# Performance work log

Hardware: AMD Instinct MI355X
Metric: run time of the kernel (lower is better)

The kernel has to match this reference:

```python
import jax, jax.numpy as jnp
import numpy as np

POOL = 7  # adaptive_avg_pool2d output size (7,7)


def _bin_edges(start, length):
    """Adaptive-avg-pool bin boundaries.
    start, length: [N] int32 -> (lo, hi) each [N, POOL] absolute indices,
    matching torch: lo_i = floor(i*L/P), hi_i = ceil((i+1)*L/P).
    """
    i = jnp.arange(POOL, dtype=jnp.int32)
    lo = start[:, None] + (i[None, :] * length[:, None]) // POOL
    hi = start[:, None] + (-((-(i[None, :] + 1)) * length[:, None] // POOL))
    # note: ceil(a/b) = -(-a // b); written below explicitly
    hi = start[:, None] - ((-(i[None, :] + 1) * length[:, None]) // POOL)
    return lo, hi


def roi_adaptive_avg_pool(features, rois):
    """features: [1, C, H, W]; rois: [N, 4] int (x1,y1,x2,y2 inclusive).
    Returns [N, C, POOL, POOL] == torch stack of adaptive_avg_pool2d over
    features[:, :, y1:y2+1, x1:x2+1], vectorized via an integral image.
    """
    B, C, H, W = features.shape  # B == 1 (forced by shared_fcs input dim)
    # integral image with a zero row/col prepended: ii[y, x] = sum over [:y, :x]
    ii = jnp.cumsum(jnp.cumsum(features, axis=2), axis=3)
    ii = jnp.pad(ii, ((0, 0), (0, 0), (1, 0), (1, 0)))[0]  # [C, H+1, W+1]

    x1, y1, x2, y2 = rois[:, 0], rois[:, 1], rois[:, 2], rois[:, 3]
    ys, ye = _bin_edges(y1, y2 - y1 + 1)   # [N, POOL]
    xs, xe = _bin_edges(x1, x2 - x1 + 1)
    Y0, Y1 = ys[:, :, None], ye[:, :, None]   # [N, POOL, 1]
    X0, X1 = xs[:, None, :], xe[:, None, :]   # [N, 1, POOL]

    def gather(Y, X):
        return ii[:, Y, X]  # [C, N, POOL, POOL]

    sums = gather(Y1, X1) - gather(Y0, X1) - gather(Y1, X0) + gather(Y0, X0)
    area = ((Y1 - Y0) * (X1 - X0)).astype(features.dtype)  # [N, POOL, POOL]
    pooled = sums / area[None]                              # [C, N, POOL, POOL]
    return jnp.transpose(pooled, (1, 0, 2, 3))              # [N, C, POOL, POOL]


def setup_inputs() -> dict:
    key = jax.random.key(0)
    ks = jax.random.split(key, 12)
    C, H, W, N, F = 256, 336, 336, 2000, 256
    features = jax.random.normal(ks[0], (1, C, H, W), dtype=jnp.float32)
    # valid small ROIs (shuttlecock-sized), x1<=x2, y1<=y2, in-bounds
    x1 = jax.random.randint(ks[1], (N,), 0, W - 40)
    y1 = jax.random.randint(ks[2], (N,), 0, H - 40)
    bw = jax.random.randint(ks[3], (N,), 4, 40)
    bh = jax.random.randint(ks[4], (N,), 4, 40)
    rois = jnp.stack([x1, y1, jnp.minimum(x1 + bw, W - 1),
                      jnp.minimum(y1 + bh, H - 1)], axis=1).astype(jnp.int32)
    d_in = C * POOL * POOL
    w1 = jax.random.normal(ks[5], (d_in, F), dtype=jnp.float32) * (1.0 / np.sqrt(d_in))
    b1 = jnp.zeros((F,), dtype=jnp.float32)
    w2 = jax.random.normal(ks[6], (F, F), dtype=jnp.float32) * (1.0 / np.sqrt(F))
    b2 = jnp.zeros((F,), dtype=jnp.float32)
    w_cls = jax.random.normal(ks[7], (F, 2), dtype=jnp.float32) * 0.01
    b_cls = jnp.zeros((2,), dtype=jnp.float32)
    w_reg = jax.random.normal(ks[8], (F, 4), dtype=jnp.float32) * 0.001
    b_reg = jnp.zeros((4,), dtype=jnp.float32)
    return {"features": features, "rois": rois, "w1": w1, "b1": b1,
            "w2": w2, "b2": b2, "w_cls": w_cls, "b_cls": b_cls,
            "w_reg": w_reg, "b_reg": b_reg}


def reference(features, rois, w1, b1, w2, b2, w_cls, b_cls, w_reg, b_reg):
    roi_feats = roi_adaptive_avg_pool(features, rois)          # [N, C, 7, 7]
    roi_feats = roi_feats.reshape(roi_feats.shape[0], -1)      # [N, C*49]
    h = jax.nn.relu(roi_feats @ w1 + b1)
    h = jax.nn.relu(h @ w2 + b2)
    cls_score = h @ w_cls + b_cls                              # [N, num_classes+1]
    bbox_pred = h @ w_reg + b_reg                              # [N, 4]
    return (cls_score, bbox_pred)
```

## Files before the change

kernel.cpp:

```cpp
#include <hip/hip_runtime.h>

typedef unsigned int uint;
typedef unsigned short ushort;
typedef __bf16 v8bf __attribute__((ext_vector_type(8)));
typedef float v4f __attribute__((ext_vector_type(4)));

#define CCH 256
#define HH 336
#define WW 336
#define HWSZ (HH*WW)
#define NROI 2000
#define KDIM 12544
#define MPAD 2048
#define SPLITK 14
#define KSP (KDIM/SPLITK)

__device__ __forceinline__ ushort bf16r(float f) {
  uint u = __float_as_uint(f);
  u += 0x7fffu + ((u >> 16) & 1u);
  return (ushort)(u >> 16);
}
__device__ __forceinline__ uint packbf(float a, float b) {
  return (uint)bf16r(a) | ((uint)bf16r(b) << 16);
}

typedef const __attribute__((address_space(1))) uint* gas_t;
typedef __attribute__((address_space(3))) uint* las_t;
__device__ __forceinline__ void async16(const void* g, void* l) {
  __builtin_amdgcn_global_load_lds((gas_t)g, (las_t)l, 16, 0, 0);
}

__global__ __launch_bounds__(256) void k_transpose(const float* __restrict__ f,
                                                   uint* __restrict__ ftu) {
  __shared__ uint T[64 * 132];
  int tid = threadIdx.x;
  int hw0 = blockIdx.x * 64;
  int hwl = tid & 63;
  int cq = tid >> 6;
  int hw = hw0 + hwl;
#pragma unroll 4
  for (int it = 0; it < 32; ++it) {
    int c = it * 8 + cq * 2;
    float a = f[(size_t)c * HWSZ + hw];
    float b = f[(size_t)(c + 1) * HWSZ + hw];
    T[hwl * 132 + it * 4 + cq] = packbf(a, b);
  }
  __syncthreads();
  int co = tid & 31, r = tid >> 5;
#pragma unroll
  for (int i = 0; i < 8; ++i) {
    int hwr = i * 8 + r;
    uint4 v = *(const uint4*)&T[hwr * 132 + co * 4];
    *(uint4*)(ftu + (size_t)(hw0 + hwr) * 128 + co * 4) = v;
  }
}

__global__ __launch_bounds__(256) void k_w1perm(const float* __restrict__ w1,
                                                uint* __restrict__ w1t_u) {
  int bin = blockIdx.x % 49;
  int c0 = (blockIdx.x / 49) * 32;
  __shared__ ushort T[32][258];
  int n = threadIdx.x;
  for (int i = 0; i < 32; ++i)
    T[i][n] = bf16r(w1[(size_t)((c0 + i) * 49 + bin) * 256 + n]);
  __syncthreads();
  int cc = threadIdx.x & 15;
  int nb = threadIdx.x >> 4;
  for (int rep = 0; rep < 16; ++rep) {
    int nn = rep * 16 + nb;
    uint v = (uint)T[2 * cc][nn] | ((uint)T[2 * cc + 1][nn] << 16);
    w1t_u[(size_t)nn * (KDIM / 2) + bin * 128 + c0 / 2 + cc] = v;
  }
}

__global__ __launch_bounds__(256) void k_w2t(const float* __restrict__ w2,
                                             ushort* __restrict__ w2t) {
  int n = blockIdx.x, k = threadIdx.x;
  w2t[n * 256 + k] = bf16r(w2[k * 256 + n]);
}

#define UNPK8(u) do {                                        \
  a[0] += __uint_as_float((u).x << 16);                      \
  a[1] += __uint_as_float((u).x & 0xffff0000u);              \
  a[2] += __uint_as_float((u).y << 16);                      \
  a[3] += __uint_as_float((u).y & 0xffff0000u);              \
  a[4] += __uint_as_float((u).z << 16);                      \
  a[5] += __uint_as_float((u).z & 0xffff0000u);              \
  a[6] += __uint_as_float((u).w << 16);                      \
  a[7] += __uint_as_float((u).w & 0xffff0000u);              \
} while (0)

__global__ __launch_bounds__(448) void k_pool(const int* __restrict__ rois,
                                              const uint4* __restrict__ ft4,
                                              uint4* __restrict__ rf4) {
  int n = blockIdx.x;
  int wv = threadIdx.x >> 6;
  int t = threadIdx.x & 63;
  int co = t & 31, par = t >> 5;
  int x1 = rois[n * 4 + 0], y1 = rois[n * 4 + 1];
  int x2 = rois[n * 4 + 2], y2 = rois[n * 4 + 3];
  int Lw = x2 - x1 + 1, Lh = y2 - y1 + 1;
  int ylo = y1 + (wv * Lh) / 7;
  int yhi = y1 + ((wv + 1) * Lh + 6) / 7;
  int rh = yhi - ylo;
  uint ob = (uint)n * 1568 + (uint)wv * 224 + co;
  for (int b = 0; b < 7; ++b) {
    int lo = x1 + (b * Lw) / 7;
    int hi = x1 + ((b + 1) * Lw + 6) / 7;
    float a[8];
#pragma unroll
    for (int j = 0; j < 8; ++j) a[j] = 0.f;
    for (int y = ylo; y < yhi; ++y) {
      const uint4* p = ft4 + (size_t)(y * WW + lo + par) * 32 + co;
      for (int x = lo + par; x < hi; x += 2) {
        uint4 u = *p; p += 64;
        UNPK8(u);
      }
    }
#pragma unroll
    for (int j = 0; j < 8; ++j) a[j] += __shfl_xor(a[j], 32, 64);
    if (t < 32) {
      float inv = 1.0f / (float)(rh * (hi - lo));
      uint4 o;
      o.x = packbf(a[0] * inv, a[1] * inv);
      o.y = packbf(a[2] * inv, a[3] * inv);
      o.z = packbf(a[4] * inv, a[5] * inv);
      o.w = packbf(a[6] * inv, a[7] * inv);
      rf4[ob + b * 32] = o;
    }
  }
}

__global__ __launch_bounds__(256) void k_gemm1(const ushort* __restrict__ A,
                                               const ushort* __restrict__ B,
                                               float* __restrict__ P) {
  __shared__ ushort As[128 * 64];
  __shared__ ushort Bs[64 * 64];
  int m0 = blockIdx.x * 128;
  int n0 = blockIdx.y * 64;
  int ks = blockIdx.z;
  int k0 = ks * KSP;
  int tid = threadIdx.x;
  int lane = tid & 63, wv = tid >> 6;
  int wm = wv & 1, wn = wv >> 1;
  int lm = lane & 15, quad = lane >> 4;
  int srow = tid >> 3, scol = (tid & 7) * 8;
  v4f acc[4][2];
#pragma unroll
  for (int i = 0; i < 4; ++i)
#pragma unroll
    for (int j = 0; j < 2; ++j) acc[i][j] = (v4f){0.f, 0.f, 0.f, 0.f};
  const ushort* Ab = A + (size_t)(m0 + srow) * KDIM + k0 + scol;
  const ushort* Bb = B + (size_t)(n0 + srow) * KDIM + k0 + scol;
  for (int kt = 0; kt < KSP / 64; ++kt) {
    __syncthreads();
#pragma unroll
    for (int r = 0; r < 4; ++r)
      async16(Ab + (size_t)(r * 32) * KDIM + kt * 64, &As[(srow + r * 32) * 64 + scol]);
#pragma unroll
    for (int r = 0; r < 2; ++r)
      async16(Bb + (size_t)(r * 32) * KDIM + kt * 64, &Bs[(srow + r * 32) * 64 + scol]);
    __syncthreads();
#pragma unroll
    for (int kk = 0; kk < 64; kk += 32) {
      v8bf a[4], b[2];
#pragma unroll
      for (int i = 0; i < 4; ++i)
        a[i] = *(const v8bf*)&As[(wm * 64 + i * 16 + lm) * 64 + kk + quad * 8];
#pragma unroll
      for (int j = 0; j < 2; ++j)
        b[j] = *(const v8bf*)&Bs[(wn * 32 + j * 16 + lm) * 64 + kk + quad * 8];
#pragma unroll
      for (int i = 0; i < 4; ++i)
#pragma unroll
        for (int j = 0; j < 2; ++j)
          acc[i][j] = __builtin_amdgcn_mfma_f32_16x16x32_bf16(a[i], b[j], acc[i][j], 0, 0, 0);
    }
  }
  float* Pb = P + (size_t)ks * MPAD * 256;
#pragma unroll
  for (int i = 0; i < 4; ++i)
#pragma unroll
    for (int j = 0; j < 2; ++j) {
      int row = m0 + wm * 64 + i * 16 + quad * 4;
      int col = n0 + wn * 32 + j * 16 + lm;
#pragma unroll
      for (int r = 0; r < 4; ++r)
        Pb[(size_t)(row + r) * 256 + col] = acc[i][j][r];
    }
}

__global__ __launch_bounds__(256) void k_reduce(const float* __restrict__ P,
                                                const float* __restrict__ b1,
                                                uint* __restrict__ h1u) {
  int idx = blockIdx.x * 256 + threadIdx.x;
  int m = idx >> 7, np = idx & 127;
  const float2* Pp = (const float2*)P;
  float2 s = {0.f, 0.f};
#pragma unroll
  for (int ks = 0; ks < SPLITK; ++ks) {
    float2 v = Pp[(size_t)(ks * MPAD + m) * 128 + np];
    s.x += v.x; s.y += v.y;
  }
  s.x += b1[2 * np]; s.y += b1[2 * np + 1];
  s.x = fmaxf(s.x, 0.f); s.y = fmaxf(s.y, 0.f);
  h1u[idx] = packbf(s.x, s.y);
}

__global__ __launch_bounds__(256) void k_gemm2(const ushort* __restrict__ h1b,
                                               const ushort* __restrict__ w2t,
                                               const float* __restrict__ b2,
                                               const float* __restrict__ wcls,
                                               const float* __restrict__ bcls,
                                               const float* __restrict__ wreg,
                                               const float* __restrict__ breg,
                                               float* __restrict__ out) {
  __shared__ ushort As2[64 * 64];
  __shared__ ushort Bs2[256 * 64];
  __shared__ float Hs[64 * 257];
  int tid = threadIdx.x;
  int r0 = blockIdx.x * 64;
  int lane = tid & 63, wv = tid >> 6;
  int lm = lane & 15, quad = lane >> 4;
  int srow = tid >> 3, scol = (tid & 7) * 8;
  v4f acc[16];
#pragma unroll
  for (int j = 0; j < 16; ++j) acc[j] = (v4f){0.f, 0.f, 0.f, 0.f};
  for (int kt = 0; kt < 4; ++kt) {
    __syncthreads();
#pragma unroll
    for (int r = 0; r < 2; ++r)
      async16(h1b + (size_t)(r0 + srow + r * 32) * 256 + kt * 64 + scol,
              &As2[(srow + r * 32) * 64 + scol]);
#pragma unroll
    for (int r = 0; r < 8; ++r)
      async16(w2t + (size_t)(srow + r * 32) * 256 + kt * 64 + scol,
              &Bs2[(srow + r * 32) * 64 + scol]);
    __syncthreads();
#pragma unroll
    for (int kk = 0; kk < 64; kk += 32) {
      v8bf a = *(const v8bf*)&As2[(wv * 16 + lm) * 64 + kk + quad * 8];
#pragma unroll
      for (int j = 0; j < 16; ++j) {
        v8bf b = *(const v8bf*)&Bs2[(j * 16 + lm) * 64 + kk + quad * 8];
        acc[j] = __builtin_amdgcn_mfma_f32_16x16x32_bf16(a, b, acc[j], 0, 0, 0);
      }
    }
  }
#pragma unroll
  for (int j = 0; j < 16; ++j) {
    int nn = j * 16 + lm;
    float bb = b2[nn];
#pragma unroll
    for (int r = 0; r < 4; ++r) {
      int row = wv * 16 + quad * 4 + r;
      Hs[row * 257 + nn] = fmaxf(acc[j][r] + bb, 0.f);
    }
  }
  __syncthreads();
  for (int o = tid; o < 384; o += 256) {
    int hd = o >> 6, r = o & 63;
    int grow = r0 + r;
    float d = 0.f;
    if (hd < 2) {
      for (int k = 0; k < 256; ++k) d += Hs[r * 257 + k] * wcls[k * 2 + hd];
      d += bcls[hd];
      if (grow < NROI) out[grow * 2 + hd] = d;
    } else {
      int h4 = hd - 2;
      for (int k = 0; k < 256; ++k) d += Hs[r * 257 + k] * wreg[k * 4 + h4];
      d += breg[h4];
      if (grow < NROI) out[4000 + grow * 4 + h4] = d;
    }
  }
}

extern "C" void kernel_launch(void* const* d_in, const int* in_sizes, int n_in,
                              void* d_out, int out_size, void* d_ws, size_t ws_size,
                              hipStream_t stream) {
  const float* features = (const float*)d_in[0];
  const int* rois = (const int*)d_in[1];
  const float* w1 = (const float*)d_in[2];
  const float* b1 = (const float*)d_in[3];
  const float* w2 = (const float*)d_in[4];
  const float* b2 = (const float*)d_in[5];
  const float* wcls = (const float*)d_in[6];
  const float* bcls = (const float*)d_in[7];
  const float* wreg = (const float*)d_in[8];
  const float* breg = (const float*)d_in[9];
  char* ws = (char*)d_ws;
  ushort* ft  = (ushort*)(ws + 0);
  ushort* w1t = (ushort*)(ws + 57802752);
  ushort* w2t = (ushort*)(ws + 64225280);
  ushort* rf  = (ushort*)(ws + 64356352);
  float*  P   = (float*)(ws + 115736576);
  ushort* h1b = (ushort*)(ws + 145096704);
  float* out = (float*)d_out;

  hipLaunchKernelGGL(k_transpose, dim3(HWSZ / 64), dim3(256), 0, stream,
                     features, (uint*)ft);
  hipLaunchKernelGGL(k_w1perm, dim3(392), dim3(256), 0, stream, w1, (uint*)w1t);
  hipLaunchKernelGGL(k_w2t, dim3(256), dim3(256), 0, stream, w2, w2t);
  hipLaunchKernelGGL(k_pool, dim3(NROI), dim3(448), 0, stream, rois,
                     (const uint4*)ft, (uint4*)rf);
  hipLaunchKernelGGL(k_gemm1, dim3(16, 4, SPLITK), dim3(256), 0, stream, rf, w1t, P);
  hipLaunchKernelGGL(k_reduce, dim3(1024), dim3(256), 0, stream, P, b1, (uint*)h1b);
  hipLaunchKernelGGL(k_gemm2, dim3(32), dim3(256), 0, stream, h1b, w2t, b2, wcls, bcls, wreg, breg, out);
}
```

Baseline: 397.4 us.

## Sort ROIs by spatial bucket and remap pool blocks for L2 locality

Adds a single-block counting-sort kernel that buckets ROIs by centre into an 8x8 spatial grid and writes a permutation. The pooling kernel then reads its ROI through this permutation, with block indices swizzled across the eight XCDs so that spatially close ROIs run on the same XCD and share feature rows in its L2. This costs an extra serial launch plus a tiny sort, and adds an indirection for the pooled output rows.

```diff
diff --git a/kernel.cpp b/kernel.cpp
--- a/kernel.cpp
+++ b/kernel.cpp
@@ -79,6 +79,33 @@
   w2t[n * 256 + k] = bf16r(w2[k * 256 + n]);
 }
 
+__global__ __launch_bounds__(256) void k_sort(const int* __restrict__ rois,
+                                              int* __restrict__ perm) {
+  __shared__ int hist[64];
+  __shared__ int keys[NROI];
+  int tid = threadIdx.x;
+  if (tid < 64) hist[tid] = 0;
+  __syncthreads();
+  for (int i = tid; i < NROI; i += 256) {
+    int x1 = rois[i * 4 + 0], y1 = rois[i * 4 + 1];
+    int x2 = rois[i * 4 + 2], y2 = rois[i * 4 + 3];
+    int cx = (x1 + x2) >> 1, cy = (y1 + y2) >> 1;
+    int k = (cy / 42) * 8 + (cx / 42);
+    keys[i] = k;
+    atomicAdd(&hist[k], 1);
+  }
+  __syncthreads();
+  if (tid == 0) {
+    int s = 0;
+    for (int b = 0; b < 64; ++b) { int c = hist[b]; hist[b] = s; s += c; }
+  }
+  __syncthreads();
+  for (int i = tid; i < NROI; i += 256) {
+    int pos = atomicAdd(&hist[keys[i]], 1);
+    perm[pos] = i;
+  }
+}
+
 #define UNPK8(u) do {                                        \
   a[0] += __uint_as_float((u).x << 16);                      \
   a[1] += __uint_as_float((u).x & 0xffff0000u);              \
@@ -91,9 +118,11 @@
 } while (0)
 
 __global__ __launch_bounds__(448) void k_pool(const int* __restrict__ rois,
+                                              const int* __restrict__ perm,
                                               const uint4* __restrict__ ft4,
                                               uint4* __restrict__ rf4) {
-  int n = blockIdx.x;
+  int slot = (blockIdx.x & 7) * 250 + (blockIdx.x >> 3);
+  int n = perm[slot];
   int wv = threadIdx.x >> 6;
   int t = threadIdx.x & 63;
   int co = t & 31, par = t >> 5;
@@ -293,6 +322,7 @@
   ushort* w1t = (ushort*)(ws + 57802752);
   ushort* w2t = (ushort*)(ws + 64225280);
   ushort* rf  = (ushort*)(ws + 64356352);
+  int*    perm = (int*)(ws + 64356352 + (size_t)NROI * KDIM * 2);
   float*  P   = (float*)(ws + 115736576);
   ushort* h1b = (ushort*)(ws + 145096704);
   float* out = (float*)d_out;
@@ -301,7 +331,8 @@
                      features, (uint*)ft);
   hipLaunchKernelGGL(k_w1perm, dim3(392), dim3(256), 0, stream, w1, (uint*)w1t);
   hipLaunchKernelGGL(k_w2t, dim3(256), dim3(256), 0, stream, w2, w2t);
-  hipLaunchKernelGGL(k_pool, dim3(NROI), dim3(448), 0, stream, rois,
+  hipLaunchKernelGGL(k_sort, dim3(1), dim3(256), 0, stream, rois, perm);
+  hipLaunchKernelGGL(k_pool, dim3(NROI), dim3(448), 0, stream, rois, perm,
                      (const uint4*)ft, (uint4*)rf);
   hipLaunchKernelGGL(k_gemm1, dim3(16, 4, SPLITK), dim3(256), 0, stream, rf, w1t, P);
   hipLaunchKernelGGL(k_reduce, dim3(1024), dim3(256), 0, stream, P, b1, (uint*)h1b);
```

After: 370.4 us. 1.07x faster.
